# Kernel optimization log

Hardware: AMD Instinct MI355X
Metric: run time of the kernel (lower is better)

Reference implementation:

```python
import jax, jax.numpy as jnp
import numpy as np

B = 64          # batch of graphs
N_GOALS = 16
N_SHELVES = 112
N = N_GOALS + N_SHELVES   # 128 nodes per graph
L = 5           # num_layers
D = 32          # node_embedding_dim
DE = 32         # edge_embedding_dim
DT = 32         # timestep_embedding_dim
D_MSG_IN = 2 * D + DT + 1  # 97


def setup_inputs() -> dict:
    key = jax.random.key(0)
    ks = iter(jax.random.split(key, 40))
    def nrm(shape, s=0.05):
        return jax.random.normal(next(ks), shape, jnp.float32) * s
    inp = {}
    inp["pos"] = jax.random.uniform(next(ks), (B, N_SHELVES, 2), jnp.float32, -1.0, 1.0)
    inp["timesteps"] = jax.random.randint(next(ks), (B,), 0, 1000)
    inp["goal_pos"] = jax.random.uniform(next(ks), (N_GOALS, 2), jnp.float32, -1.0, 1.0)
    inp["W_hin"] = nrm((2, D));            inp["b_hin"] = nrm((D,))
    inp["W_msg1"] = nrm((L, D_MSG_IN, DE)); inp["b_msg1"] = nrm((L, DE))
    inp["W_msg2"] = nrm((L, DE, DE));       inp["b_msg2"] = nrm((L, DE))
    inp["W_att"] = nrm((L, DE, 1));         inp["b_att"] = nrm((L, 1))
    inp["W_pos1"] = nrm((L, DE, DE));       inp["b_pos1"] = nrm((L, DE))
    inp["W_pos2"] = nrm((L, DE, 1));        inp["b_pos2"] = nrm((L, 1))
    inp["W_node1"] = nrm((L - 1, DE + D, D)); inp["b_node1"] = nrm((L - 1, D))
    inp["W_node2"] = nrm((L - 1, D, D));      inp["b_node2"] = nrm((L - 1, D))
    inp["W_t"] = nrm((L - 1, DT, DT));        inp["b_t"] = nrm((L - 1, DT))
    return inp


def _forward(pos, timesteps, goal_pos, W_hin, b_hin, W_msg1, b_msg1, W_msg2, b_msg2,
             W_att, b_att, W_pos1, b_pos1, W_pos2, b_pos2,
             W_node1, b_node1, W_node2, b_node2, W_t, b_t):
    silu = jax.nn.silu
    b = pos.shape[0]
    n_g = goal_pos.shape[0]
    n_sh = pos.shape[1]
    n = n_g + n_sh
    num_layers = W_msg1.shape[0]

    # fully-connected edge template per graph (PyG: edge_index[0]=src=row, edge_index[1]=dst=col)
    src_l = jnp.repeat(jnp.arange(n), n)
    dst_l = jnp.tile(jnp.arange(n), n)
    offs = (jnp.arange(b) * n)[:, None]
    src = (offs + src_l[None, :]).reshape(-1)   # [b*n*n]
    dst = (offs + dst_l[None, :]).reshape(-1)
    e_batch = jnp.repeat(jnp.arange(b), n * n)  # batch[edge_index[0]]

    # node one-hot features: goals [1,0], shelves [0,1]
    h0 = jnp.concatenate([
        jnp.tile(jnp.array([1.0, 0.0], jnp.float32), (n_g, 1)),
        jnp.tile(jnp.array([0.0, 1.0], jnp.float32), (n_sh, 1)),
    ], axis=0)                                   # [n, 2]
    x = jnp.tile(h0, (b, 1))                     # [b*n, 2]

    # node positions: goal positions (shared template) then shelf positions
    p = jnp.concatenate([jnp.broadcast_to(goal_pos, (b, n_g, 2)), pos], axis=1).reshape(-1, 2)

    # sinusoidal timestep embedding
    dt = b_t.shape[-1]
    half = dt // 2
    freqs = jnp.exp(-jnp.log(10000.0) * jnp.arange(half, dtype=jnp.float32) / half)
    ang = timesteps.astype(jnp.float32)[:, None] * freqs[None, :]
    temb = jnp.concatenate([jnp.cos(ang), jnp.sin(ang)], axis=-1)  # [b, dt]

    h = x @ W_hin + b_hin  # [b*n, D]

    for i in range(num_layers):
        te = temb[e_batch]                       # [E, dt]
        pd = p[dst] - p[src]                     # pos_i - pos_j
        radial = jnp.sum(pd * pd, axis=-1, keepdims=True)
        pd = pd / (jax.lax.stop_gradient(jnp.sqrt(radial)) + 1e-6)
        m = jnp.concatenate([h[dst], h[src], radial, te], axis=-1)  # [E, 97]
        m = silu(m @ W_msg1[i] + b_msg1[i])
        m = silu(m @ W_msg2[i] + b_msg2[i])
        m = m * jax.nn.sigmoid(m @ W_att[i] + b_att[i])             # attention gate
        pw = silu(m @ W_pos1[i] + b_pos1[i]) @ W_pos2[i] + b_pos2[i]  # [E, 1]
        aggr_h = jax.ops.segment_sum(m, dst, num_segments=b * n)    # scatter-add
        # scatter-mean: every node receives exactly n incoming edges (fully connected incl. self-loop)
        aggr_p = jax.ops.segment_sum(pd * pw, dst, num_segments=b * n) / n
        if i < num_layers - 1:
            u = silu(jnp.concatenate([h, aggr_h], axis=-1) @ W_node1[i] + b_node1[i])
            u = u @ W_node2[i] + b_node2[i]
            h = jnp.where(u > 0, u, 0.01 * u) + h   # LeakyReLU + residual
            temb = silu(temb @ W_t[i] + b_t[i])
        p = aggr_p + p

    return p.reshape(b, n, 2)[:, n_g:, :].reshape(pos.shape)


def reference(pos, timesteps, goal_pos, W_hin, b_hin, W_msg1, b_msg1, W_msg2, b_msg2,
              W_att, b_att, W_pos1, b_pos1, W_pos2, b_pos2,
              W_node1, b_node1, W_node2, b_node2, W_t, b_t):
    return _forward(pos, timesteps, goal_pos, W_hin, b_hin, W_msg1, b_msg1, W_msg2, b_msg2,
                    W_att, b_att, W_pos1, b_pos1, W_pos2, b_pos2,
                    W_node1, b_node1, W_node2, b_node2, W_t, b_t)
```

## Files before the change

kernel.cpp:

```cpp
#include <hip/hip_runtime.h>
#include <hip/hip_bf16.h>

constexpr int B = 64;
constexpr int NG = 16;
constexpr int NSH = 112;
constexpr int N = 128;
constexpr int NN = B * N;
constexpr int L = 5;

constexpr int OFF_H     = 0;
constexpr int OFF_P0    = OFF_H + NN * 32;
constexpr int OFF_P1    = OFF_P0 + NN * 2;
constexpr int OFF_TEMB0 = OFF_P1 + NN * 2;
constexpr int OFF_TEMB1 = OFF_TEMB0 + B * 32;
constexpr int OFF_HA0   = OFF_TEMB1 + B * 32;
constexpr int OFF_HA1   = OFF_HA0 + NN * 32;
constexpr int OFF_HB0   = OFF_HA1 + NN * 32;
constexpr int OFF_HB1   = OFF_HB0 + NN * 16;

typedef __attribute__((ext_vector_type(8))) short bf16x8;
typedef __attribute__((ext_vector_type(4))) float f32x4;

__device__ __forceinline__ float fsigmoid(float x) {
    return __builtin_amdgcn_rcpf(1.0f + __expf(-x));
}
__device__ __forceinline__ float fsilu(float x) { return x * fsigmoid(x); }
__device__ __forceinline__ short f2bfs(float f) {
    union { __hip_bfloat16 b; short s; } u; u.b = __float2bfloat16(f); return u.s;
}
__device__ __forceinline__ float bf2f(unsigned short u) {
    union { unsigned int i; float f; } v; v.i = ((unsigned int)u) << 16; return v.f;
}
__device__ __forceinline__ unsigned int pk_trunc(float lo, float hi) {
    union { float f; unsigned int u; } a, b;
    a.f = hi; b.f = lo;
    return __builtin_amdgcn_perm(a.u, b.u, 0x07060302u);
}

__global__ __launch_bounds__(256) void setup_pre_kernel(
    float* __restrict__ ws,
    const float* __restrict__ pos, const int* __restrict__ tsteps,
    const float* __restrict__ goal_pos,
    const float* __restrict__ W_hin, const float* __restrict__ b_hin,
    const float* __restrict__ W_msg1, const float* __restrict__ b_msg1)
{
    __shared__ float sT[32];
    const int t = threadIdx.x, bx = blockIdx.x;
    const int tid = bx * 256 + t;
    const int c = tid & 31, node = tid >> 5, g = node >> 7, local = node & 127;
    const int row = (local < NG) ? 0 : 1;

    if (t < 32) {
        const float tf = (float)tsteps[g];
        const int jj = (t < 16) ? t : (t - 16);
        const float ang = tf * expf(-logf(10000.0f) * (float)jj / 16.0f);
        sT[t] = (t < 16) ? cosf(ang) : sinf(ang);
    }
    __syncthreads();
    if ((bx & 15) == 0 && t < 32) ws[OFF_TEMB0 + g * 32 + t] = sT[t];

    ws[OFF_H + tid] = W_hin[row * 32 + c] + b_hin[c];

    if (tid < NN * 2) {
        const int d = tid & 1, nd = tid >> 1, g0 = nd >> 7, loc = nd & 127;
        ws[OFF_P0 + tid] = (loc < NG) ? goal_pos[loc * 2 + d]
                                      : pos[(g0 * NSH + (loc - NG)) * 2 + d];
    }

    const float* __restrict__ W1 = W_msg1;
    float accA = b_msg1[c], accB = 0.f;
#pragma unroll
    for (int k = 0; k < 32; ++k) {
        const float hk = W_hin[row * 32 + k] + b_hin[k];
        accA += hk * W1[k * 32 + c];
        accB += hk * W1[(32 + k) * 32 + c];
    }
#pragma unroll
    for (int k = 0; k < 32; ++k)
        accA += sT[k] * W1[(65 + k) * 32 + c];
    ws[OFF_HA0 + tid] = accA;
    ((unsigned short*)(ws + OFF_HB0))[tid] = (unsigned short)f2bfs(accB);
}

__global__ __attribute__((amdgpu_flat_work_group_size(256, 256)))
__attribute__((amdgpu_waves_per_eu(2, 4))) void edge_kernel(
    float* __restrict__ ws,
    const float* __restrict__ W_msg1, const float* __restrict__ b_msg1,
    const float* __restrict__ W_msg2, const float* __restrict__ b_msg2,
    const float* __restrict__ W_att, const float* __restrict__ b_att,
    const float* __restrict__ W_pos1, const float* __restrict__ b_pos1,
    const float* __restrict__ W_pos2, const float* __restrict__ b_pos2,
    const float* __restrict__ W_node1, const float* __restrict__ b_node1,
    const float* __restrict__ W_node2, const float* __restrict__ b_node2,
    const float* __restrict__ W_t, const float* __restrict__ b_t,
    float* __restrict__ out, int l)
{
    __shared__ unsigned short sHBh[128 * 40];
    __shared__ float sPx[128], sPy[128];
    __shared__ __align__(16) unsigned char uraw[14336];
    __shared__ float sAgg[16][36];
    __shared__ float2 sAgp[16];

    unsigned int* mbuf = (unsigned int*)uraw;
    float2* spn = (float2*)(uraw + 10240);
    float (*sH)[36] = (float(*)[36])uraw;
    unsigned int* nmb = (unsigned int*)(uraw + 2304);

    const int t = threadIdx.x;
    const int bx = blockIdx.x;
    const int g = bx >> 4, qp = bx & 15;
    const int gbase = g << 7;
    const int par = l & 1, op = (l + 1) & 1;

    const float* __restrict__ HAin = ws + (par ? OFF_HA1 : OFF_HA0);
    const unsigned short* __restrict__ HBin = (const unsigned short*)(ws + (par ? OFF_HB1 : OFF_HB0));
    const float* __restrict__ Pin = ws + (par ? OFF_P1 : OFF_P0);

#pragma unroll
    for (int ch = 0; ch < 2; ++ch) {
        const int chunk = t + (ch << 8);
        const int row = chunk >> 2, g4 = chunk & 3;
        *(uint4*)(sHBh + row * 40 + (g4 << 3)) =
            *(const uint4*)(HBin + (gbase + row) * 32 + (g4 << 3));
    }
    if (t < 128) {
        sPx[t] = Pin[(gbase + t) * 2];
        sPy[t] = Pin[(gbase + t) * 2 + 1];
    }
    __syncthreads();

    const int lane = t & 63, w = t >> 6;
    const int c = lane & 15, rg = lane >> 4, kk = rg << 3;

    const float* __restrict__ Wm2L = W_msg2 + l * 1024;
    const float* __restrict__ Wp1L = W_pos1 + l * 1024;
    bf16x8 WB1c0, WB1c1, WBpc0, WBpc1, WBac;
#pragma unroll
    for (int j = 0; j < 8; ++j) {
        WB1c0[j] = f2bfs(Wm2L[(kk + j) * 32 + c]);
        WB1c1[j] = f2bfs(Wm2L[(kk + j) * 32 + c + 16]);
        const int pk = ((kk + j) & 1) * 16 + ((kk + j) >> 1);
        WBpc0[j] = f2bfs(Wp1L[pk * 32 + c]);
        WBpc1[j] = f2bfs(Wp1L[pk * 32 + c + 16]);
        WBac[j]  = f2bfs(W_att[l * 32 + pk]);
    }
    float vwr[8];
    {
        const float* wrR = W_msg1 + l * 97 * 32 + 64 * 32 + kk;
#pragma unroll
        for (int j = 0; j < 8; ++j) vwr[j] = wrR[j];
    }
    const float batt  = b_att[l];
    const float vbm20 = b_msg2[l * 32 + c], vbm21 = b_msg2[l * 32 + c + 16];
    const float vbp10 = b_pos1[l * 32 + c], vbp11 = b_pos1[l * 32 + c + 16];
    const float vwp20 = W_pos2[l * 32 + c], vwp21 = W_pos2[l * 32 + c + 16];
    const float bp2   = b_pos2[l];

    unsigned int* mbA = mbuf + w * 320;
    unsigned int* mbB = mbuf + (w + 4) * 320;

    const int dlA = w, dlB = w + 4;
    const int dlocA = (qp << 3) + dlA, dlocB = (qp << 3) + dlB;
    float vhaA[8], vhaB[8];
    {
        const float* haRA = HAin + (gbase + dlocA) * 32 + kk;
        const float* haRB = HAin + (gbase + dlocB) * 32 + kk;
#pragma unroll
        for (int j = 0; j < 8; ++j) { vhaA[j] = haRA[j]; vhaB[j] = haRB[j]; }
    }
    const float pxdA = sPx[dlocA], pydA = sPy[dlocA];
    const float pxdB = sPx[dlocB], pydB = sPy[dlocB];

    float aghc0A = 0.f, aghc1A = 0.f, apxA = 0.f, apyA = 0.f, spnxA = 0.f, spnyA = 0.f;
    float aghc0B = 0.f, aghc1B = 0.f, apxB = 0.f, apyB = 0.f, spnxB = 0.f, spnyB = 0.f;

#pragma unroll 1
    for (int half = 0; half < 2; ++half) {
        const int src = (half << 6) + lane;
        const float sx = sPx[src], sy = sPy[src];
        const float dxA = pxdA - sx, dyA = pydA - sy;
        const float dxB = pxdB - sx, dyB = pydB - sy;
        const float radialA = dxA * dxA + dyA * dyA;
        const float radialB = dxB * dxB + dyB * dyB;
        const float invA = __builtin_amdgcn_rcpf(__builtin_amdgcn_sqrtf(radialA) + 1e-6f);
        const float invB = __builtin_amdgcn_rcpf(__builtin_amdgcn_sqrtf(radialB) + 1e-6f);
        const float pnxA = dxA * invA, pnyA = dyA * invA;
        const float pnxB = dxB * invB, pnyB = dyB * invB;
        spnxA += pnxA; spnyA += pnyA;
        spnxB += pnxB; spnyB += pnyB;
        spn[w * 64 + lane]       = (float2){pnxA, pnyA};
        spn[(w + 4) * 64 + lane] = (float2){pnxB, pnyB};

#pragma unroll
        for (int tt = 0; tt < 4; ++tt) {
            const float rad_tA = __shfl(radialA, c + (tt << 4));
            const float rad_tB = __shfl(radialB, c + (tt << 4));
            uint4 hraw = *(const uint4*)(sHBh + ((half << 6) + c + (tt << 4)) * 40 + kk);
            const unsigned short* hs = (const unsigned short*)&hraw;
            float xA[8], xB[8];
#pragma unroll
            for (int j = 0; j < 8; ++j) {
                const float hb = bf2f(hs[j]);
                xA[j] = fsilu(vhaA[j] + hb + rad_tA * vwr[j]);
                xB[j] = fsilu(vhaB[j] + hb + rad_tB * vwr[j]);
            }
            union { unsigned int u[4]; bf16x8 v; } afA, afB;
#pragma unroll
            for (int d = 0; d < 4; ++d) {
                afA.u[d] = pk_trunc(xA[2 * d], xA[2 * d + 1]);
                afB.u[d] = pk_trunc(xB[2 * d], xB[2 * d + 1]);
            }
            f32x4 a0A = (f32x4){vbm20, vbm20, vbm20, vbm20};
            f32x4 a1A = (f32x4){vbm21, vbm21, vbm21, vbm21};
            f32x4 a0B = a0A, a1B = a1A;
            a0A = __builtin_amdgcn_mfma_f32_16x16x32_bf16(afA.v, WB1c0, a0A, 0, 0, 0);
            a1A = __builtin_amdgcn_mfma_f32_16x16x32_bf16(afA.v, WB1c1, a1A, 0, 0, 0);
            a0B = __builtin_amdgcn_mfma_f32_16x16x32_bf16(afB.v, WB1c0, a0B, 0, 0, 0);
            a1B = __builtin_amdgcn_mfma_f32_16x16x32_bf16(afB.v, WB1c1, a1B, 0, 0, 0);

            float s0A[4], s1A[4], s0B[4], s1B[4];
#pragma unroll
            for (int j = 0; j < 4; ++j) {
                s0A[j] = fsilu(a0A[j]);
                s1A[j] = fsilu(a1A[j]);
                s0B[j] = fsilu(a0B[j]);
                s1B[j] = fsilu(a1B[j]);
                mbA[((rg << 2) + j) * 20 + c] = pk_trunc(s0A[j], s1A[j]);
                mbB[((rg << 2) + j) * 20 + c] = pk_trunc(s0B[j], s1B[j]);
            }

            union { uint4 u; bf16x8 v; } qaA, qaB;
            qaA.u = *(const uint4*)(mbA + c * 20 + (rg << 2));
            qaB.u = *(const uint4*)(mbB + c * 20 + (rg << 2));
            f32x4 zaA = (f32x4){batt, batt, batt, batt};
            f32x4 zaB = zaA;
            f32x4 z0A = (f32x4){0.f, 0.f, 0.f, 0.f};
            f32x4 z1A = z0A, z0B = z0A, z1B = z0A;
            zaA = __builtin_amdgcn_mfma_f32_16x16x32_bf16(qaA.v, WBac,  zaA, 0, 0, 0);
            z0A = __builtin_amdgcn_mfma_f32_16x16x32_bf16(qaA.v, WBpc0, z0A, 0, 0, 0);
            z1A = __builtin_amdgcn_mfma_f32_16x16x32_bf16(qaA.v, WBpc1, z1A, 0, 0, 0);
            zaB = __builtin_amdgcn_mfma_f32_16x16x32_bf16(qaB.v, WBac,  zaB, 0, 0, 0);
            z0B = __builtin_amdgcn_mfma_f32_16x16x32_bf16(qaB.v, WBpc0, z0B, 0, 0, 0);
            z1B = __builtin_amdgcn_mfma_f32_16x16x32_bf16(qaB.v, WBpc1, z1B, 0, 0, 0);
#pragma unroll
            for (int j = 0; j < 4; ++j) {
                const float attA = fsigmoid(zaA[j]);
                const float attB = fsigmoid(zaB[j]);
                aghc0A += attA * s0A[j];
                aghc1A += attA * s1A[j];
                aghc0B += attB * s0B[j];
                aghc1B += attB * s1B[j];
                const float q0A = fsilu(attA * z0A[j] + vbp10);
                const float q1A = fsilu(attA * z1A[j] + vbp11);
                const float q0B = fsilu(attB * z0B[j] + vbp10);
                const float q1B = fsilu(attB * z1B[j] + vbp11);
                const float pwpA = q0A * vwp20 + q1A * vwp21;
                const float pwpB = q0B * vwp20 + q1B * vwp21;
                const float2 pnA = spn[w * 64 + (tt << 4) + (rg << 2) + j];
                const float2 pnB = spn[(w + 4) * 64 + (tt << 4) + (rg << 2) + j];
                apxA += pwpA * pnA.x;
                apyA += pwpA * pnA.y;
                apxB += pwpB * pnB.x;
                apyB += pwpB * pnB.y;
            }
        }
    }

    aghc0A += __shfl_xor(aghc0A, 16); aghc0A += __shfl_xor(aghc0A, 32);
    aghc1A += __shfl_xor(aghc1A, 16); aghc1A += __shfl_xor(aghc1A, 32);
    aghc0B += __shfl_xor(aghc0B, 16); aghc0B += __shfl_xor(aghc0B, 32);
    aghc1B += __shfl_xor(aghc1B, 16); aghc1B += __shfl_xor(aghc1B, 32);
#pragma unroll
    for (int off = 1; off < 64; off <<= 1) {
        apxA  += __shfl_xor(apxA, off);
        apyA  += __shfl_xor(apyA, off);
        spnxA += __shfl_xor(spnxA, off);
        spnyA += __shfl_xor(spnyA, off);
        apxB  += __shfl_xor(apxB, off);
        apyB  += __shfl_xor(apyB, off);
        spnxB += __shfl_xor(spnxB, off);
        spnyB += __shfl_xor(spnyB, off);
    }
    if (l < L - 1) {
        if (lane < 32) {
            sAgg[dlA][lane] = (lane < 16) ? aghc0A : aghc1A;
            sAgg[dlB][lane] = (lane < 16) ? aghc0B : aghc1B;
        }
        if (lane == 0) {
            sAgp[dlA] = (float2){(apxA + bp2 * spnxA) * (1.0f / 128.0f),
                                 (apyA + bp2 * spnyA) * (1.0f / 128.0f)};
            sAgp[dlB] = (float2){(apxB + bp2 * spnxB) * (1.0f / 128.0f),
                                 (apyB + bp2 * spnyB) * (1.0f / 128.0f)};
        }
    } else if (lane == 0) {
        if (dlocA >= NG) {
            out[(g * NSH + (dlocA - NG)) * 2]     = pxdA + (apxA + bp2 * spnxA) * (1.0f / 128.0f);
            out[(g * NSH + (dlocA - NG)) * 2 + 1] = pydA + (apyA + bp2 * spnyA) * (1.0f / 128.0f);
        }
        if (dlocB >= NG) {
            out[(g * NSH + (dlocB - NG)) * 2]     = pxdB + (apxB + bp2 * spnxB) * (1.0f / 128.0f);
            out[(g * NSH + (dlocB - NG)) * 2 + 1] = pydB + (apyB + bp2 * spnyB) * (1.0f / 128.0f);
        }
    }
    if (l == L - 1) return;

    __syncthreads();

    if (t < 64) {
        const int nbase = bx << 3;
        float* __restrict__ HAout = ws + (op ? OFF_HA1 : OFF_HA0);
        unsigned short* __restrict__ HBout = (unsigned short*)(ws + (op ? OFF_HB1 : OFF_HB0));
        float* __restrict__ Pout = ws + (op ? OFF_P1 : OFF_P0);

        {
            const int row8 = lane >> 3, seg = lane & 7;
            const float* hsrc = ws + OFF_H + (nbase + row8) * 32 + (seg << 2);
#pragma unroll
            for (int j = 0; j < 4; ++j) sH[row8][(seg << 2) + j] = hsrc[j];
        }

        const float* __restrict__ Wn1 = W_node1 + l * 2048;
        const float* __restrict__ Wn2 = W_node2 + l * 1024;
        const float* __restrict__ W1  = W_msg1 + (l + 1) * 97 * 32;
        bf16x8 B1[2][2], B2[2], Ba[2], Bb[2];
#pragma unroll
        for (int j = 0; j < 8; ++j) {
            const int pk = ((kk + j) & 1) * 16 + ((kk + j) >> 1);
#pragma unroll
            for (int nh = 0; nh < 2; ++nh) {
                B1[0][nh][j] = f2bfs(Wn1[(kk + j) * 32 + nh * 16 + c]);
                B1[1][nh][j] = f2bfs(Wn1[(32 + kk + j) * 32 + nh * 16 + c]);
                B2[nh][j]    = f2bfs(Wn2[pk * 32 + nh * 16 + c]);
                Ba[nh][j]    = f2bfs(W1[pk * 32 + nh * 16 + c]);
                Bb[nh][j]    = f2bfs(W1[(32 + pk) * 32 + nh * 16 + c]);
            }
        }

        const int c2 = lane & 31;
        const float* __restrict__ tin = ws + (par ? OFF_TEMB1 : OFF_TEMB0) + g * 32;
        const float* __restrict__ Wt = W_t + l * 1024;
        float a2 = b_t[l * 32 + c2];
#pragma unroll
        for (int k = 0; k < 32; ++k) a2 += tin[k] * Wt[k * 32 + c2];
        const float tnew = fsilu(a2);
        float tv = b_msg1[(l + 1) * 32 + c2];
#pragma unroll
        for (int k = 0; k < 32; ++k) tv += __shfl(tnew, k) * W1[(65 + k) * 32 + c2];
        if ((bx & 15) == 0 && lane < 32)
            ws[(par ? OFF_TEMB0 : OFF_TEMB1) + g * 32 + lane] = tnew;

        union { unsigned int u[4]; bf16x8 v; } A0, A1;
#pragma unroll
        for (int d = 0; d < 4; ++d) {
            A0.u[d] = pk_trunc(sH[c][kk + 2 * d],   sH[c][kk + 2 * d + 1]);
            A1.u[d] = pk_trunc(sAgg[c][kk + 2 * d], sAgg[c][kk + 2 * d + 1]);
        }
        f32x4 u1[2];
#pragma unroll
        for (int nh = 0; nh < 2; ++nh) {
            const float bb = b_node1[l * 32 + nh * 16 + c];
            f32x4 acc = (f32x4){bb, bb, bb, bb};
            acc = __builtin_amdgcn_mfma_f32_16x16x32_bf16(A0.v, B1[0][nh], acc, 0, 0, 0);
            acc = __builtin_amdgcn_mfma_f32_16x16x32_bf16(A1.v, B1[1][nh], acc, 0, 0, 0);
            u1[nh] = acc;
        }

#pragma unroll
        for (int j = 0; j < 4; ++j)
            nmb[((rg << 2) + j) * 20 + c] = pk_trunc(fsilu(u1[0][j]), fsilu(u1[1][j]));
        union { uint4 q; bf16x8 v; } qa;
        qa.q = *(const uint4*)(nmb + c * 20 + (rg << 2));
        f32x4 u2[2];
#pragma unroll
        for (int nh = 0; nh < 2; ++nh) {
            const float bb = b_node2[l * 32 + nh * 16 + c];
            f32x4 acc = (f32x4){bb, bb, bb, bb};
            u2[nh] = __builtin_amdgcn_mfma_f32_16x16x32_bf16(qa.v, B2[nh], acc, 0, 0, 0);
        }

        float hp0[4], hp1[4];
#pragma unroll
        for (int j = 0; j < 4; ++j) {
            const int row = (rg << 2) + j;
            const float h0 = sH[row][c], h1 = sH[row][c + 16];
            const float v0 = u2[0][j], v1 = u2[1][j];
            hp0[j] = (v0 > 0.f ? v0 : 0.01f * v0) + h0;
            hp1[j] = (v1 > 0.f ? v1 : 0.01f * v1) + h1;
            if (row < 8) {
                ws[OFF_H + (nbase + row) * 32 + c]      = hp0[j];
                ws[OFF_H + (nbase + row) * 32 + c + 16] = hp1[j];
            }
            nmb[row * 20 + c] = pk_trunc(hp0[j], hp1[j]);
        }

        qa.q = *(const uint4*)(nmb + c * 20 + (rg << 2));
        f32x4 ha[2], hb[2];
        {
            f32x4 zz = (f32x4){0.f, 0.f, 0.f, 0.f};
#pragma unroll
            for (int nh = 0; nh < 2; ++nh) {
                ha[nh] = __builtin_amdgcn_mfma_f32_16x16x32_bf16(qa.v, Ba[nh], zz, 0, 0, 0);
                hb[nh] = __builtin_amdgcn_mfma_f32_16x16x32_bf16(qa.v, Bb[nh], zz, 0, 0, 0);
            }
        }
        const float tv0 = __shfl(tv, c), tv1 = __shfl(tv, c + 16);
#pragma unroll
        for (int j = 0; j < 4; ++j) {
            const int row = (rg << 2) + j;
            if (row < 8) {
                const int node = nbase + row;
                HAout[node * 32 + c]      = ha[0][j] + tv0;
                HAout[node * 32 + c + 16] = ha[1][j] + tv1;
                HBout[node * 32 + c]      = (unsigned short)f2bfs(hb[0][j]);
                HBout[node * 32 + c + 16] = (unsigned short)f2bfs(hb[1][j]);
            }
        }

        if (lane < 16) {
            const int dl2 = lane >> 1, d = lane & 1;
            const int node = nbase + dl2;
            const float ag = d ? sAgp[dl2].y : sAgp[dl2].x;
            Pout[node * 2 + d] = (par ? ws[OFF_P1 + node * 2 + d]
                                      : ws[OFF_P0 + node * 2 + d]) + ag;
        }
    }
}

extern "C" void kernel_launch(void* const* d_in, const int* in_sizes, int n_in,
                              void* d_out, int out_size, void* d_ws, size_t ws_size,
                              hipStream_t stream)
{
    const float* pos      = (const float*)d_in[0];
    const int*   tsteps   = (const int*)d_in[1];
    const float* goal_pos = (const float*)d_in[2];
    const float* W_hin    = (const float*)d_in[3];
    const float* b_hin    = (const float*)d_in[4];
    const float* W_msg1   = (const float*)d_in[5];
    const float* b_msg1   = (const float*)d_in[6];
    const float* W_msg2   = (const float*)d_in[7];
    const float* b_msg2   = (const float*)d_in[8];
    const float* W_att    = (const float*)d_in[9];
    const float* b_att    = (const float*)d_in[10];
    const float* W_pos1   = (const float*)d_in[11];
    const float* b_pos1   = (const float*)d_in[12];
    const float* W_pos2   = (const float*)d_in[13];
    const float* b_pos2   = (const float*)d_in[14];
    const float* W_node1  = (const float*)d_in[15];
    const float* b_node1  = (const float*)d_in[16];
    const float* W_node2  = (const float*)d_in[17];
    const float* b_node2  = (const float*)d_in[18];
    const float* W_t      = (const float*)d_in[19];
    const float* b_t      = (const float*)d_in[20];

    float* ws = (float*)d_ws;

    setup_pre_kernel<<<1024, 256, 0, stream>>>(ws, pos, tsteps, goal_pos,
                                               W_hin, b_hin, W_msg1, b_msg1);

    for (int l = 0; l < L; ++l)
        edge_kernel<<<1024, 256, 0, stream>>>(ws, W_msg1, b_msg1, W_msg2, b_msg2,
                                              W_att, b_att, W_pos1, b_pos1,
                                              W_pos2, b_pos2, W_node1, b_node1,
                                              W_node2, b_node2, W_t, b_t,
                                              (float*)d_out, l);
}
```

Measured before the change: 290.2 us.

## Process 32 destination nodes per block with four-block grid per graph

Each block now handles 32 destination nodes, looping four times over groups of 8, instead of 8 nodes per block, so the grid shrinks from 1024 to 256 blocks. The per-block staging of HB and positions into shared memory and the weight fragment setup are amortised over more destinations. The node-update epilogue now runs two full 16-row MFMA tiles, where before it ran one half-used tile. The cost is fewer blocks: 256 blocks on a 256-CU part gives roughly one block per CU, which lowers occupancy and latency hiding.

```diff
diff --git a/kernel.cpp b/kernel.cpp
--- a/kernel.cpp
+++ b/kernel.cpp
@@ -98,8 +98,8 @@
     __shared__ unsigned short sHBh[128 * 40];
     __shared__ float sPx[128], sPy[128];
     __shared__ __align__(16) unsigned char uraw[14336];
-    __shared__ float sAgg[16][36];
-    __shared__ float2 sAgp[16];
+    __shared__ float sAgg[32][36];
+    __shared__ float2 sAgp[32];
 
     unsigned int* mbuf = (unsigned int*)uraw;
     float2* spn = (float2*)(uraw + 10240);
@@ -108,7 +108,7 @@
 
     const int t = threadIdx.x;
     const int bx = blockIdx.x;
-    const int g = bx >> 4, qp = bx & 15;
+    const int g = bx >> 2, qp = bx & 3;
     const int gbase = g << 7;
     const int par = l & 1, op = (l + 1) & 1;
 
@@ -159,147 +159,150 @@
     unsigned int* mbA = mbuf + w * 320;
     unsigned int* mbB = mbuf + (w + 4) * 320;
 
-    const int dlA = w, dlB = w + 4;
-    const int dlocA = (qp << 3) + dlA, dlocB = (qp << 3) + dlB;
-    float vhaA[8], vhaB[8];
-    {
-        const float* haRA = HAin + (gbase + dlocA) * 32 + kk;
-        const float* haRB = HAin + (gbase + dlocB) * 32 + kk;
-#pragma unroll
-        for (int j = 0; j < 8; ++j) { vhaA[j] = haRA[j]; vhaB[j] = haRB[j]; }
-    }
-    const float pxdA = sPx[dlocA], pydA = sPy[dlocA];
-    const float pxdB = sPx[dlocB], pydB = sPy[dlocB];
-
-    float aghc0A = 0.f, aghc1A = 0.f, apxA = 0.f, apyA = 0.f, spnxA = 0.f, spnyA = 0.f;
-    float aghc0B = 0.f, aghc1B = 0.f, apxB = 0.f, apyB = 0.f, spnxB = 0.f, spnyB = 0.f;
-
 #pragma unroll 1
-    for (int half = 0; half < 2; ++half) {
-        const int src = (half << 6) + lane;
-        const float sx = sPx[src], sy = sPy[src];
-        const float dxA = pxdA - sx, dyA = pydA - sy;
-        const float dxB = pxdB - sx, dyB = pydB - sy;
-        const float radialA = dxA * dxA + dyA * dyA;
-        const float radialB = dxB * dxB + dyB * dyB;
-        const float invA = __builtin_amdgcn_rcpf(__builtin_amdgcn_sqrtf(radialA) + 1e-6f);
-        const float invB = __builtin_amdgcn_rcpf(__builtin_amdgcn_sqrtf(radialB) + 1e-6f);
-        const float pnxA = dxA * invA, pnyA = dyA * invA;
-        const float pnxB = dxB * invB, pnyB = dyB * invB;
-        spnxA += pnxA; spnyA += pnyA;
-        spnxB += pnxB; spnyB += pnyB;
-        spn[w * 64 + lane]       = (float2){pnxA, pnyA};
-        spn[(w + 4) * 64 + lane] = (float2){pnxB, pnyB};
-
-#pragma unroll
-        for (int tt = 0; tt < 4; ++tt) {
-            const float rad_tA = __shfl(radialA, c + (tt << 4));
-            const float rad_tB = __shfl(radialB, c + (tt << 4));
-            uint4 hraw = *(const uint4*)(sHBh + ((half << 6) + c + (tt << 4)) * 40 + kk);
-            const unsigned short* hs = (const unsigned short*)&hraw;
-            float xA[8], xB[8];
-#pragma unroll
-            for (int j = 0; j < 8; ++j) {
-                const float hb = bf2f(hs[j]);
-                xA[j] = fsilu(vhaA[j] + hb + rad_tA * vwr[j]);
-                xB[j] = fsilu(vhaB[j] + hb + rad_tB * vwr[j]);
-            }
-            union { unsigned int u[4]; bf16x8 v; } afA, afB;
-#pragma unroll
-            for (int d = 0; d < 4; ++d) {
-                afA.u[d] = pk_trunc(xA[2 * d], xA[2 * d + 1]);
-                afB.u[d] = pk_trunc(xB[2 * d], xB[2 * d + 1]);
-            }
-            f32x4 a0A = (f32x4){vbm20, vbm20, vbm20, vbm20};
-            f32x4 a1A = (f32x4){vbm21, vbm21, vbm21, vbm21};
-            f32x4 a0B = a0A, a1B = a1A;
-            a0A = __builtin_amdgcn_mfma_f32_16x16x32_bf16(afA.v, WB1c0, a0A, 0, 0, 0);
-            a1A = __builtin_amdgcn_mfma_f32_16x16x32_bf16(afA.v, WB1c1, a1A, 0, 0, 0);
-            a0B = __builtin_amdgcn_mfma_f32_16x16x32_bf16(afB.v, WB1c0, a0B, 0, 0, 0);
-            a1B = __builtin_amdgcn_mfma_f32_16x16x32_bf16(afB.v, WB1c1, a1B, 0, 0, 0);
-
-            float s0A[4], s1A[4], s0B[4], s1B[4];
-#pragma unroll
-            for (int j = 0; j < 4; ++j) {
-                s0A[j] = fsilu(a0A[j]);
-                s1A[j] = fsilu(a1A[j]);
-                s0B[j] = fsilu(a0B[j]);
-                s1B[j] = fsilu(a1B[j]);
-                mbA[((rg << 2) + j) * 20 + c] = pk_trunc(s0A[j], s1A[j]);
-                mbB[((rg << 2) + j) * 20 + c] = pk_trunc(s0B[j], s1B[j]);
-            }
-
-            union { uint4 u; bf16x8 v; } qaA, qaB;
-            qaA.u = *(const uint4*)(mbA + c * 20 + (rg << 2));
-            qaB.u = *(const uint4*)(mbB + c * 20 + (rg << 2));
-            f32x4 zaA = (f32x4){batt, batt, batt, batt};
-            f32x4 zaB = zaA;
-            f32x4 z0A = (f32x4){0.f, 0.f, 0.f, 0.f};
-            f32x4 z1A = z0A, z0B = z0A, z1B = z0A;
-            zaA = __builtin_amdgcn_mfma_f32_16x16x32_bf16(qaA.v, WBac,  zaA, 0, 0, 0);
-            z0A = __builtin_amdgcn_mfma_f32_16x16x32_bf16(qaA.v, WBpc0, z0A, 0, 0, 0);
-            z1A = __builtin_amdgcn_mfma_f32_16x16x32_bf16(qaA.v, WBpc1, z1A, 0, 0, 0);
-            zaB = __builtin_amdgcn_mfma_f32_16x16x32_bf16(qaB.v, WBac,  zaB, 0, 0, 0);
-            z0B = __builtin_amdgcn_mfma_f32_16x16x32_bf16(qaB.v, WBpc0, z0B, 0, 0, 0);
-            z1B = __builtin_amdgcn_mfma_f32_16x16x32_bf16(qaB.v, WBpc1, z1B, 0, 0, 0);
-#pragma unroll
-            for (int j = 0; j < 4; ++j) {
-                const float attA = fsigmoid(zaA[j]);
-                const float attB = fsigmoid(zaB[j]);
-                aghc0A += attA * s0A[j];
-                aghc1A += attA * s1A[j];
-                aghc0B += attB * s0B[j];
-                aghc1B += attB * s1B[j];
-                const float q0A = fsilu(attA * z0A[j] + vbp10);
-                const float q1A = fsilu(attA * z1A[j] + vbp11);
-                const float q0B = fsilu(attB * z0B[j] + vbp10);
-                const float q1B = fsilu(attB * z1B[j] + vbp11);
-                const float pwpA = q0A * vwp20 + q1A * vwp21;
-                const float pwpB = q0B * vwp20 + q1B * vwp21;
-                const float2 pnA = spn[w * 64 + (tt << 4) + (rg << 2) + j];
-                const float2 pnB = spn[(w + 4) * 64 + (tt << 4) + (rg << 2) + j];
-                apxA += pwpA * pnA.x;
-                apyA += pwpA * pnA.y;
-                apxB += pwpB * pnB.x;
-                apyB += pwpB * pnB.y;
-            }
-        }
-    }
-
-    aghc0A += __shfl_xor(aghc0A, 16); aghc0A += __shfl_xor(aghc0A, 32);
-    aghc1A += __shfl_xor(aghc1A, 16); aghc1A += __shfl_xor(aghc1A, 32);
-    aghc0B += __shfl_xor(aghc0B, 16); aghc0B += __shfl_xor(aghc0B, 32);
-    aghc1B += __shfl_xor(aghc1B, 16); aghc1B += __shfl_xor(aghc1B, 32);
-#pragma unroll
-    for (int off = 1; off < 64; off <<= 1) {
-        apxA  += __shfl_xor(apxA, off);
-        apyA  += __shfl_xor(apyA, off);
-        spnxA += __shfl_xor(spnxA, off);
-        spnyA += __shfl_xor(spnyA, off);
-        apxB  += __shfl_xor(apxB, off);
-        apyB  += __shfl_xor(apyB, off);
-        spnxB += __shfl_xor(spnxB, off);
-        spnyB += __shfl_xor(spnyB, off);
-    }
-    if (l < L - 1) {
-        if (lane < 32) {
-            sAgg[dlA][lane] = (lane < 16) ? aghc0A : aghc1A;
-            sAgg[dlB][lane] = (lane < 16) ? aghc0B : aghc1B;
-        }
-        if (lane == 0) {
-            sAgp[dlA] = (float2){(apxA + bp2 * spnxA) * (1.0f / 128.0f),
-                                 (apyA + bp2 * spnyA) * (1.0f / 128.0f)};
-            sAgp[dlB] = (float2){(apxB + bp2 * spnxB) * (1.0f / 128.0f),
-                                 (apyB + bp2 * spnyB) * (1.0f / 128.0f)};
-        }
-    } else if (lane == 0) {
-        if (dlocA >= NG) {
-            out[(g * NSH + (dlocA - NG)) * 2]     = pxdA + (apxA + bp2 * spnxA) * (1.0f / 128.0f);
-            out[(g * NSH + (dlocA - NG)) * 2 + 1] = pydA + (apyA + bp2 * spnyA) * (1.0f / 128.0f);
-        }
-        if (dlocB >= NG) {
-            out[(g * NSH + (dlocB - NG)) * 2]     = pxdB + (apxB + bp2 * spnxB) * (1.0f / 128.0f);
-            out[(g * NSH + (dlocB - NG)) * 2 + 1] = pydB + (apyB + bp2 * spnyB) * (1.0f / 128.0f);
+    for (int si = 0; si < 4; ++si) {
+        const int dlAl = (si << 2) + w, dlBl = dlAl + 16;
+        const int dlocA = (qp << 5) + dlAl, dlocB = (qp << 5) + dlBl;
+        float vhaA[8], vhaB[8];
+        {
+            const float* haRA = HAin + (gbase + dlocA) * 32 + kk;
+            const float* haRB = HAin + (gbase + dlocB) * 32 + kk;
+#pragma unroll
+            for (int j = 0; j < 8; ++j) { vhaA[j] = haRA[j]; vhaB[j] = haRB[j]; }
+        }
+        const float pxdA = sPx[dlocA], pydA = sPy[dlocA];
+        const float pxdB = sPx[dlocB], pydB = sPy[dlocB];
+
+        float aghc0A = 0.f, aghc1A = 0.f, apxA = 0.f, apyA = 0.f, spnxA = 0.f, spnyA = 0.f;
+        float aghc0B = 0.f, aghc1B = 0.f, apxB = 0.f, apyB = 0.f, spnxB = 0.f, spnyB = 0.f;
+
+#pragma unroll 1
+        for (int half = 0; half < 2; ++half) {
+            const int src = (half << 6) + lane;
+            const float sx = sPx[src], sy = sPy[src];
+            const float dxA = pxdA - sx, dyA = pydA - sy;
+            const float dxB = pxdB - sx, dyB = pydB - sy;
+            const float radialA = dxA * dxA + dyA * dyA;
+            const float radialB = dxB * dxB + dyB * dyB;
+            const float invA = __builtin_amdgcn_rcpf(__builtin_amdgcn_sqrtf(radialA) + 1e-6f);
+            const float invB = __builtin_amdgcn_rcpf(__builtin_amdgcn_sqrtf(radialB) + 1e-6f);
+            const float pnxA = dxA * invA, pnyA = dyA * invA;
+            const float pnxB = dxB * invB, pnyB = dyB * invB;
+            spnxA += pnxA; spnyA += pnyA;
+            spnxB += pnxB; spnyB += pnyB;
+            spn[w * 64 + lane]       = (float2){pnxA, pnyA};
+            spn[(w + 4) * 64 + lane] = (float2){pnxB, pnyB};
+
+#pragma unroll
+            for (int tt = 0; tt < 4; ++tt) {
+                const float rad_tA = __shfl(radialA, c + (tt << 4));
+                const float rad_tB = __shfl(radialB, c + (tt << 4));
+                uint4 hraw = *(const uint4*)(sHBh + ((half << 6) + c + (tt << 4)) * 40 + kk);
+                const unsigned short* hs = (const unsigned short*)&hraw;
+                float xA[8], xB[8];
+#pragma unroll
+                for (int j = 0; j < 8; ++j) {
+                    const float hb = bf2f(hs[j]);
+                    xA[j] = fsilu(vhaA[j] + hb + rad_tA * vwr[j]);
+                    xB[j] = fsilu(vhaB[j] + hb + rad_tB * vwr[j]);
+                }
+                union { unsigned int u[4]; bf16x8 v; } afA, afB;
+#pragma unroll
+                for (int d = 0; d < 4; ++d) {
+                    afA.u[d] = pk_trunc(xA[2 * d], xA[2 * d + 1]);
+                    afB.u[d] = pk_trunc(xB[2 * d], xB[2 * d + 1]);
+                }
+                f32x4 a0A = (f32x4){vbm20, vbm20, vbm20, vbm20};
+                f32x4 a1A = (f32x4){vbm21, vbm21, vbm21, vbm21};
+                f32x4 a0B = a0A, a1B = a1A;
+                a0A = __builtin_amdgcn_mfma_f32_16x16x32_bf16(afA.v, WB1c0, a0A, 0, 0, 0);
+                a1A = __builtin_amdgcn_mfma_f32_16x16x32_bf16(afA.v, WB1c1, a1A, 0, 0, 0);
+                a0B = __builtin_amdgcn_mfma_f32_16x16x32_bf16(afB.v, WB1c0, a0B, 0, 0, 0);
+                a1B = __builtin_amdgcn_mfma_f32_16x16x32_bf16(afB.v, WB1c1, a1B, 0, 0, 0);
+
+                float s0A[4], s1A[4], s0B[4], s1B[4];
+#pragma unroll
+                for (int j = 0; j < 4; ++j) {
+                    s0A[j] = fsilu(a0A[j]);
+                    s1A[j] = fsilu(a1A[j]);
+                    s0B[j] = fsilu(a0B[j]);
+                    s1B[j] = fsilu(a1B[j]);
+                    mbA[((rg << 2) + j) * 20 + c] = pk_trunc(s0A[j], s1A[j]);
+                    mbB[((rg << 2) + j) * 20 + c] = pk_trunc(s0B[j], s1B[j]);
+                }
+
+                union { uint4 u; bf16x8 v; } qaA, qaB;
+                qaA.u = *(const uint4*)(mbA + c * 20 + (rg << 2));
+                qaB.u = *(const uint4*)(mbB + c * 20 + (rg << 2));
+                f32x4 zaA = (f32x4){batt, batt, batt, batt};
+                f32x4 zaB = zaA;
+                f32x4 z0A = (f32x4){0.f, 0.f, 0.f, 0.f};
+                f32x4 z1A = z0A, z0B = z0A, z1B = z0A;
+                zaA = __builtin_amdgcn_mfma_f32_16x16x32_bf16(qaA.v, WBac,  zaA, 0, 0, 0);
+                z0A = __builtin_amdgcn_mfma_f32_16x16x32_bf16(qaA.v, WBpc0, z0A, 0, 0, 0);
+                z1A = __builtin_amdgcn_mfma_f32_16x16x32_bf16(qaA.v, WBpc1, z1A, 0, 0, 0);
+                zaB = __builtin_amdgcn_mfma_f32_16x16x32_bf16(qaB.v, WBac,  zaB, 0, 0, 0);
+                z0B = __builtin_amdgcn_mfma_f32_16x16x32_bf16(qaB.v, WBpc0, z0B, 0, 0, 0);
+                z1B = __builtin_amdgcn_mfma_f32_16x16x32_bf16(qaB.v, WBpc1, z1B, 0, 0, 0);
+#pragma unroll
+                for (int j = 0; j < 4; ++j) {
+                    const float attA = fsigmoid(zaA[j]);
+                    const float attB = fsigmoid(zaB[j]);
+                    aghc0A += attA * s0A[j];
+                    aghc1A += attA * s1A[j];
+                    aghc0B += attB * s0B[j];
+                    aghc1B += attB * s1B[j];
+                    const float q0A = fsilu(attA * z0A[j] + vbp10);
+                    const float q1A = fsilu(attA * z1A[j] + vbp11);
+                    const float q0B = fsilu(attB * z0B[j] + vbp10);
+                    const float q1B = fsilu(attB * z1B[j] + vbp11);
+                    const float pwpA = q0A * vwp20 + q1A * vwp21;
+                    const float pwpB = q0B * vwp20 + q1B * vwp21;
+                    const float2 pnA = spn[w * 64 + (tt << 4) + (rg << 2) + j];
+                    const float2 pnB = spn[(w + 4) * 64 + (tt << 4) + (rg << 2) + j];
+                    apxA += pwpA * pnA.x;
+                    apyA += pwpA * pnA.y;
+                    apxB += pwpB * pnB.x;
+                    apyB += pwpB * pnB.y;
+                }
+            }
+        }
+
+        aghc0A += __shfl_xor(aghc0A, 16); aghc0A += __shfl_xor(aghc0A, 32);
+        aghc1A += __shfl_xor(aghc1A, 16); aghc1A += __shfl_xor(aghc1A, 32);
+        aghc0B += __shfl_xor(aghc0B, 16); aghc0B += __shfl_xor(aghc0B, 32);
+        aghc1B += __shfl_xor(aghc1B, 16); aghc1B += __shfl_xor(aghc1B, 32);
+#pragma unroll
+        for (int off = 1; off < 64; off <<= 1) {
+            apxA  += __shfl_xor(apxA, off);
+            apyA  += __shfl_xor(apyA, off);
+            spnxA += __shfl_xor(spnxA, off);
+            spnyA += __shfl_xor(spnyA, off);
+            apxB  += __shfl_xor(apxB, off);
+            apyB  += __shfl_xor(apyB, off);
+            spnxB += __shfl_xor(spnxB, off);
+            spnyB += __shfl_xor(spnyB, off);
+        }
+        if (l < L - 1) {
+            if (lane < 32) {
+                sAgg[dlAl][lane] = (lane < 16) ? aghc0A : aghc1A;
+                sAgg[dlBl][lane] = (lane < 16) ? aghc0B : aghc1B;
+            }
+            if (lane == 0) {
+                sAgp[dlAl] = (float2){(apxA + bp2 * spnxA) * (1.0f / 128.0f),
+                                      (apyA + bp2 * spnyA) * (1.0f / 128.0f)};
+                sAgp[dlBl] = (float2){(apxB + bp2 * spnxB) * (1.0f / 128.0f),
+                                      (apyB + bp2 * spnyB) * (1.0f / 128.0f)};
+            }
+        } else if (lane == 0) {
+            if (dlocA >= NG) {
+                out[(g * NSH + (dlocA - NG)) * 2]     = pxdA + (apxA + bp2 * spnxA) * (1.0f / 128.0f);
+                out[(g * NSH + (dlocA - NG)) * 2 + 1] = pydA + (apyA + bp2 * spnyA) * (1.0f / 128.0f);
+            }
+            if (dlocB >= NG) {
+                out[(g * NSH + (dlocB - NG)) * 2]     = pxdB + (apxB + bp2 * spnxB) * (1.0f / 128.0f);
+                out[(g * NSH + (dlocB - NG)) * 2 + 1] = pydB + (apyB + bp2 * spnyB) * (1.0f / 128.0f);
+            }
         }
     }
     if (l == L - 1) return;
@@ -307,17 +310,9 @@
     __syncthreads();
 
     if (t < 64) {
-        const int nbase = bx << 3;
         float* __restrict__ HAout = ws + (op ? OFF_HA1 : OFF_HA0);
         unsigned short* __restrict__ HBout = (unsigned short*)(ws + (op ? OFF_HB1 : OFF_HB0));
         float* __restrict__ Pout = ws + (op ? OFF_P1 : OFF_P0);
-
-        {
-            const int row8 = lane >> 3, seg = lane & 7;
-            const float* hsrc = ws + OFF_H + (nbase + row8) * 32 + (seg << 2);
-#pragma unroll
-            for (int j = 0; j < 4; ++j) sH[row8][(seg << 2) + j] = hsrc[j];
-        }
 
         const float* __restrict__ Wn1 = W_node1 + l * 2048;
         const float* __restrict__ Wn2 = W_node2 + l * 1024;
@@ -346,82 +341,90 @@
         float tv = b_msg1[(l + 1) * 32 + c2];
 #pragma unroll
         for (int k = 0; k < 32; ++k) tv += __shfl(tnew, k) * W1[(65 + k) * 32 + c2];
-        if ((bx & 15) == 0 && lane < 32)
+        if ((bx & 3) == 0 && lane < 32)
             ws[(par ? OFF_TEMB0 : OFF_TEMB1) + g * 32 + lane] = tnew;
-
-        union { unsigned int u[4]; bf16x8 v; } A0, A1;
-#pragma unroll
-        for (int d = 0; d < 4; ++d) {
-            A0.u[d] = pk_trunc(sH[c][kk + 2 * d],   sH[c][kk + 2 * d + 1]);
-            A1.u[d] = pk_trunc(sAgg[c][kk + 2 * d], sAgg[c][kk + 2 * d + 1]);
-        }
-        f32x4 u1[2];
-#pragma unroll
-        for (int nh = 0; nh < 2; ++nh) {
-            const float bb = b_node1[l * 32 + nh * 16 + c];
-            f32x4 acc = (f32x4){bb, bb, bb, bb};
-            acc = __builtin_amdgcn_mfma_f32_16x16x32_bf16(A0.v, B1[0][nh], acc, 0, 0, 0);
-            acc = __builtin_amdgcn_mfma_f32_16x16x32_bf16(A1.v, B1[1][nh], acc, 0, 0, 0);
-            u1[nh] = acc;
-        }
-
-#pragma unroll
-        for (int j = 0; j < 4; ++j)
-            nmb[((rg << 2) + j) * 20 + c] = pk_trunc(fsilu(u1[0][j]), fsilu(u1[1][j]));
-        union { uint4 q; bf16x8 v; } qa;
-        qa.q = *(const uint4*)(nmb + c * 20 + (rg << 2));
-        f32x4 u2[2];
-#pragma unroll
-        for (int nh = 0; nh < 2; ++nh) {
-            const float bb = b_node2[l * 32 + nh * 16 + c];
-            f32x4 acc = (f32x4){bb, bb, bb, bb};
-            u2[nh] = __builtin_amdgcn_mfma_f32_16x16x32_bf16(qa.v, B2[nh], acc, 0, 0, 0);
-        }
-
-        float hp0[4], hp1[4];
-#pragma unroll
-        for (int j = 0; j < 4; ++j) {
-            const int row = (rg << 2) + j;
-            const float h0 = sH[row][c], h1 = sH[row][c + 16];
-            const float v0 = u2[0][j], v1 = u2[1][j];
-            hp0[j] = (v0 > 0.f ? v0 : 0.01f * v0) + h0;
-            hp1[j] = (v1 > 0.f ? v1 : 0.01f * v1) + h1;
-            if (row < 8) {
+        const float tv0 = __shfl(tv, c), tv1 = __shfl(tv, c + 16);
+
+#pragma unroll 1
+        for (int ep = 0; ep < 2; ++ep) {
+            const int nbase = (bx << 5) + (ep << 4);
+
+            {
+                const int row = lane >> 2, seg = lane & 3;
+                const float* hsrc = ws + OFF_H + (nbase + row) * 32 + (seg << 3);
+#pragma unroll
+                for (int j = 0; j < 8; ++j) sH[row][(seg << 3) + j] = hsrc[j];
+            }
+
+            union { unsigned int u[4]; bf16x8 v; } A0, A1;
+#pragma unroll
+            for (int d = 0; d < 4; ++d) {
+                A0.u[d] = pk_trunc(sH[c][kk + 2 * d], sH[c][kk + 2 * d + 1]);
+                A1.u[d] = pk_trunc(sAgg[(ep << 4) + c][kk + 2 * d],
+                                   sAgg[(ep << 4) + c][kk + 2 * d + 1]);
+            }
+            f32x4 u1[2];
+#pragma unroll
+            for (int nh = 0; nh < 2; ++nh) {
+                const float bb = b_node1[l * 32 + nh * 16 + c];
+                f32x4 acc = (f32x4){bb, bb, bb, bb};
+                acc = __builtin_amdgcn_mfma_f32_16x16x32_bf16(A0.v, B1[0][nh], acc, 0, 0, 0);
+                acc = __builtin_amdgcn_mfma_f32_16x16x32_bf16(A1.v, B1[1][nh], acc, 0, 0, 0);
+                u1[nh] = acc;
+            }
+
+#pragma unroll
+            for (int j = 0; j < 4; ++j)
+                nmb[((rg << 2) + j) * 20 + c] = pk_trunc(fsilu(u1[0][j]), fsilu(u1[1][j]));
+            union { uint4 q; bf16x8 v; } qa;
+            qa.q = *(const uint4*)(nmb + c * 20 + (rg << 2));
+            f32x4 u2[2];
+#pragma unroll
+            for (int nh = 0; nh < 2; ++nh) {
+                const float bb = b_node2[l * 32 + nh * 16 + c];
+                f32x4 acc = (f32x4){bb, bb, bb, bb};
+                u2[nh] = __builtin_amdgcn_mfma_f32_16x16x32_bf16(qa.v, B2[nh], acc, 0, 0, 0);
+            }
+
+            float hp0[4], hp1[4];
+#pragma unroll
+            for (int j = 0; j < 4; ++j) {
+                const int row = (rg << 2) + j;
+                const float h0 = sH[row][c], h1 = sH[row][c + 16];
+                const float v0 = u2[0][j], v1 = u2[1][j];
+                hp0[j] = (v0 > 0.f ? v0 : 0.01f * v0) + h0;
+                hp1[j] = (v1 > 0.f ? v1 : 0.01f * v1) + h1;
                 ws[OFF_H + (nbase + row) * 32 + c]      = hp0[j];
                 ws[OFF_H + (nbase + row) * 32 + c + 16] = hp1[j];
-            }
-            nmb[row * 20 + c] = pk_trunc(hp0[j], hp1[j]);
-        }
-
-        qa.q = *(const uint4*)(nmb + c * 20 + (rg << 2));
-        f32x4 ha[2], hb[2];
-        {
-            f32x4 zz = (f32x4){0.f, 0.f, 0.f, 0.f};
-#pragma unroll
-            for (int nh = 0; nh < 2; ++nh) {
-                ha[nh] = __builtin_amdgcn_mfma_f32_16x16x32_bf16(qa.v, Ba[nh], zz, 0, 0, 0);
-                hb[nh] = __builtin_amdgcn_mfma_f32_16x16x32_bf16(qa.v, Bb[nh], zz, 0, 0, 0);
-            }
-        }
-        const float tv0 = __shfl(tv, c), tv1 = __shfl(tv, c + 16);
-#pragma unroll
-        for (int j = 0; j < 4; ++j) {
-            const int row = (rg << 2) + j;
-            if (row < 8) {
-                const int node = nbase + row;
+                nmb[row * 20 + c] = pk_trunc(hp0[j], hp1[j]);
+            }
+
+            qa.q = *(const uint4*)(nmb + c * 20 + (rg << 2));
+            f32x4 ha[2], hb[2];
+            {
+                f32x4 zz = (f32x4){0.f, 0.f, 0.f, 0.f};
+#pragma unroll
+                for (int nh = 0; nh < 2; ++nh) {
+                    ha[nh] = __builtin_amdgcn_mfma_f32_16x16x32_bf16(qa.v, Ba[nh], zz, 0, 0, 0);
+                    hb[nh] = __builtin_amdgcn_mfma_f32_16x16x32_bf16(qa.v, Bb[nh], zz, 0, 0, 0);
+                }
+            }
+#pragma unroll
+            for (int j = 0; j < 4; ++j) {
+                const int node = nbase + (rg << 2) + j;
                 HAout[node * 32 + c]      = ha[0][j] + tv0;
                 HAout[node * 32 + c + 16] = ha[1][j] + tv1;
                 HBout[node * 32 + c]      = (unsigned short)f2bfs(hb[0][j]);
                 HBout[node * 32 + c + 16] = (unsigned short)f2bfs(hb[1][j]);
             }
-        }
-
-        if (lane < 16) {
-            const int dl2 = lane >> 1, d = lane & 1;
-            const int node = nbase + dl2;
-            const float ag = d ? sAgp[dl2].y : sAgp[dl2].x;
-            Pout[node * 2 + d] = (par ? ws[OFF_P1 + node * 2 + d]
-                                      : ws[OFF_P0 + node * 2 + d]) + ag;
+
+            if (lane < 32) {
+                const int dl2 = lane >> 1, d = lane & 1;
+                const int node = nbase + dl2;
+                const float ag = d ? sAgp[(ep << 4) + dl2].y : sAgp[(ep << 4) + dl2].x;
+                Pout[node * 2 + d] = (par ? ws[OFF_P1 + node * 2 + d]
+                                          : ws[OFF_P0 + node * 2 + d]) + ag;
+            }
         }
     }
 }
@@ -458,9 +461,9 @@
                                                W_hin, b_hin, W_msg1, b_msg1);
 
     for (int l = 0; l < L; ++l)
-        edge_kernel<<<1024, 256, 0, stream>>>(ws, W_msg1, b_msg1, W_msg2, b_msg2,
-                                              W_att, b_att, W_pos1, b_pos1,
-                                              W_pos2, b_pos2, W_node1, b_node1,
-                                              W_node2, b_node2, W_t, b_t,
-                                              (float*)d_out, l);
-}
+        edge_kernel<<<256, 256, 0, stream>>>(ws, W_msg1, b_msg1, W_msg2, b_msg2,
+                                             W_att, b_att, W_pos1, b_pos1,
+                                             W_pos2, b_pos2, W_node1, b_node1,
+                                             W_node2, b_node2, W_t, b_t,
+                                             (float*)d_out, l);
+}
```

Result: slower. 311.0 us (+7.2%).
